# Kernel tuning notes

Measured on AMD Instinct MI355X. Metric: run time of the kernel, lower is better.

## Reference

```python
import jax, jax.numpy as jnp
import numpy as np

B, N, NFEAT = 32, 512, 256
NHID, NHEADS, NOUT = 64, 8, 128
ALPHA = 0.2    # GraphAttn LeakyReLU slope
ACVT_SLOPE = 0.01  # default nn.LeakyReLU slope in GAT.acvt
EPS = 1e-12


def _leaky(x, slope):
    return jnp.where(x >= 0, x, slope * x)


def setup_inputs() -> dict:
    key = jax.random.key(0)
    ks = jax.random.split(key, 10)
    s = lambda fan_in: 1.0 / np.sqrt(fan_in)
    return {
        "batch_descs": jax.random.normal(ks[0], (B, N, NFEAT), dtype=jnp.float32),
        # per-head GraphAttn params (nn.Linear weights, no bias)
        "W_tran": jax.random.uniform(ks[1], (NHEADS, NHID, NFEAT), jnp.float32, -s(NFEAT), s(NFEAT)),
        "a1": jax.random.uniform(ks[2], (NHEADS, NHID), jnp.float32, -s(NHID), s(NHID)),
        "a2": jax.random.uniform(ks[3], (NHEADS, NHID), jnp.float32, -s(NHID), s(NHID)),
        # output GraphAttn: in = NHID*NHEADS, out = NOUT
        "W_out": jax.random.uniform(ks[4], (NOUT, NHID * NHEADS), jnp.float32, -s(NHID * NHEADS), s(NHID * NHEADS)),
        "a1_out": jax.random.uniform(ks[5], (NOUT,), jnp.float32, -s(NOUT), s(NOUT)),
        "a2_out": jax.random.uniform(ks[6], (NOUT,), jnp.float32, -s(NOUT), s(NOUT)),
        # final nn.Linear(nout, nout) with bias
        "W_lin": jax.random.uniform(ks[7], (NOUT, NOUT), jnp.float32, -s(NOUT), s(NOUT)),
        "b_lin": jax.random.uniform(ks[8], (NOUT,), jnp.float32, -s(NOUT), s(NOUT)),
    }


def reference(batch_descs, W_tran, a1, a2, W_out, a1_out, a2_out, W_lin, b_lin):
    def gat_one_object(x):  # x: [N, NFEAT]; dense all-ones adj (ignored by GraphAttn)
        # ---- multi-head GraphAttn ----
        h = jnp.einsum('nf,hdf->hnd', x, W_tran)          # [H, N, NHID]
        e1 = jnp.einsum('hnd,hd->hn', h, a1)              # [H, N]
        e2 = jnp.einsum('hnd,hd->hn', h, a2)              # [H, N]
        # e[h, j, k] = a1(h_k) + a2(h_j); softmax over k (torch dim=1 on [N,N])
        e = _leaky(e1[:, None, :] + e2[:, :, None], ALPHA)  # [H, N, N]
        att = jax.nn.softmax(e, axis=-1)
        o = jnp.einsum('hjk,hkd->hjd', att, h)            # [H, N, NHID]
        o = jnp.transpose(o, (1, 0, 2)).reshape(N, NHEADS * NHID)  # concat heads
        # ---- acvt (dropout2 is identity in eval) ----
        x2 = _leaky(o, ACVT_SLOPE)
        # ---- output GraphAttn ----
        h2 = x2 @ W_out.T                                 # [N, NOUT]
        f1 = h2 @ a1_out                                  # [N]
        f2 = h2 @ a2_out                                  # [N]
        e_o = _leaky(f1[None, :] + f2[:, None], ALPHA)    # [N, N]
        att_o = jax.nn.softmax(e_o, axis=-1)
        out = att_o @ h2                                  # [N, NOUT]
        out = jnp.mean(out, axis=0)                       # [NOUT]
        return out @ W_lin.T + b_lin

    feats = jax.vmap(gat_one_object)(batch_descs)         # [B, NOUT]
    # F.normalize(p=2, dim=-1) with eps clamp
    norm = jnp.maximum(jnp.linalg.norm(feats, axis=-1, keepdims=True), EPS)
    return feats / norm
```

## Files before the change

kernel.cpp:

```cpp
#include <hip/hip_runtime.h>
#include <hip/hip_bf16.h>
#include <math.h>

#define ALPHA 0.2f
#define ACVT 0.01f

typedef __attribute__((ext_vector_type(8))) __bf16 bf16x8;
typedef __attribute__((ext_vector_type(4))) __bf16 bf16x4;
typedef __attribute__((ext_vector_type(4))) float f32x4;

__device__ __forceinline__ bf16x8 cvt8(const float* p) {
    float4 v0 = *(const float4*)p;
    float4 v1 = *(const float4*)(p + 4);
    bf16x8 o;
    o[0] = (__bf16)v0.x; o[1] = (__bf16)v0.y; o[2] = (__bf16)v0.z; o[3] = (__bf16)v0.w;
    o[4] = (__bf16)v1.x; o[5] = (__bf16)v1.y; o[6] = (__bf16)v1.z; o[7] = (__bf16)v1.w;
    return o;
}

__global__ __launch_bounds__(256) void gemm1_f(
    const float* __restrict__ X, const float* __restrict__ Wt,
    __bf16* __restrict__ HT,
    const float* __restrict__ a1, const float* __restrict__ a2,
    float* __restrict__ E1, float* __restrict__ E2) {
    __shared__ char As[128 * 128];
    __shared__ char Bs[128 * 128];
    __shared__ char Tt[128 * 264];
    const int tid = threadIdx.x;
    const int w = tid >> 6, lane = tid & 63;
    const int wm = w >> 1, wn = w & 1;
    const int r = lane & 15, g = lane >> 4;
    const int L = blockIdx.x;
    const int W = (L & 7) * 64 + (L >> 3);
    const int m_tile = W >> 2, n_tile = W & 3;
    const int m0 = m_tile * 128;
    const int n0 = n_tile * 128;

    f32x4 acc[4][4];
#pragma unroll
    for (int mt = 0; mt < 4; ++mt)
#pragma unroll
        for (int nt = 0; nt < 4; ++nt) {
            acc[mt][nt][0] = 0.f; acc[mt][nt][1] = 0.f;
            acc[mt][nt][2] = 0.f; acc[mt][nt][3] = 0.f;
        }

    const int sr = tid >> 3;
    const int c8 = (tid & 7) * 8;

    for (int k0 = 0; k0 < 256; k0 += 64) {
        __syncthreads();
#pragma unroll
        for (int i = 0; i < 4; ++i) {
            int row = sr + i * 32;
            bf16x8 va = cvt8(X + (size_t)(m0 + row) * 256 + k0 + c8);
            *(bf16x8*)(As + row * 128 + ((c8 * 2) ^ ((row & 7) << 4))) = va;
            bf16x8 vb = cvt8(Wt + (size_t)(n0 + row) * 256 + k0 + c8);
            *(bf16x8*)(Bs + row * 128 + ((c8 * 2) ^ ((row & 7) << 4))) = vb;
        }
        __syncthreads();
#pragma unroll
        for (int kk = 0; kk < 64; kk += 32) {
            bf16x8 af[4], bfv[4];
#pragma unroll
            for (int mt = 0; mt < 4; ++mt) {
                int row = wm * 64 + mt * 16 + r;
                af[mt] = *(const bf16x8*)(As + row * 128 +
                                          (((kk + g * 8) * 2) ^ ((row & 7) << 4)));
            }
#pragma unroll
            for (int nt = 0; nt < 4; ++nt) {
                int row = wn * 64 + nt * 16 + r;
                bfv[nt] = *(const bf16x8*)(Bs + row * 128 +
                                           (((kk + g * 8) * 2) ^ ((row & 7) << 4)));
            }
#pragma unroll
            for (int mt = 0; mt < 4; ++mt)
#pragma unroll
                for (int nt = 0; nt < 4; ++nt)
                    acc[mt][nt] = __builtin_amdgcn_mfma_f32_16x16x32_bf16(
                        af[mt], bfv[nt], acc[mt][nt], 0, 0, 0);
        }
    }

#pragma unroll
    for (int mt = 0; mt < 4; ++mt) {
        int node = wm * 64 + mt * 16 + g * 4;
#pragma unroll
        for (int nt = 0; nt < 4; ++nt) {
            int d_blk = wn * 64 + nt * 16 + r;
            bf16x4 pv;
#pragma unroll
            for (int reg = 0; reg < 4; ++reg) pv[reg] = (__bf16)acc[mt][nt][reg];
            *(bf16x4*)(Tt + d_blk * 264 + node * 2) = pv;
        }
    }
    __syncthreads();
    {
        const int b = m0 >> 9, nn = m0 & 511;
        const int h0 = n_tile * 2;
#pragma unroll
        for (int i = 0; i < 8; ++i) {
            int d_row = (tid >> 4) + i * 16;
            int hrow = (b * 8 + h0 + (d_row >> 6)) * 64 + (d_row & 63);
            bf16x8 v = *(const bf16x8*)(Tt + d_row * 264 + (tid & 15) * 16);
            *(bf16x8*)(HT + (size_t)hrow * 512 + nn + (tid & 15) * 8) = v;
        }
    }
    const int h = n_tile * 2 + wn;
    float w1[4], w2[4];
#pragma unroll
    for (int nt = 0; nt < 4; ++nt) {
        w1[nt] = a1[h * 64 + nt * 16 + r];
        w2[nt] = a2[h * 64 + nt * 16 + r];
    }
#pragma unroll
    for (int mt = 0; mt < 4; ++mt)
#pragma unroll
        for (int reg = 0; reg < 4; ++reg) {
            float s1 = 0.f, s2 = 0.f;
#pragma unroll
            for (int nt = 0; nt < 4; ++nt) {
                s1 += acc[mt][nt][reg] * w1[nt];
                s2 += acc[mt][nt][reg] * w2[nt];
            }
#pragma unroll
            for (int off = 1; off <= 8; off <<= 1) {
                s1 += __shfl_xor(s1, off, 64);
                s2 += __shfl_xor(s2, off, 64);
            }
            if (r == 0) {
                int m = m0 + wm * 64 + mt * 16 + g * 4 + reg;
                int b = m >> 9, n = m & 511;
                E1[(size_t)(b * 8 + h) * 512 + n] = s1;
                E2[(size_t)(b * 8 + h) * 512 + n] = s2;
            }
        }
}

__global__ __launch_bounds__(256) void attn_s(const __bf16* __restrict__ HT,
                                              const float* __restrict__ E1,
                                              const float* __restrict__ E2,
                                              __bf16* __restrict__ OL) {
    __shared__ char Hc[4096];
    __shared__ float e1s[512];
    __shared__ float redm[256];
    __shared__ float zrow[4][32];
    __shared__ float e1maxS;

    const int bid = blockIdx.x;
    const int bh = bid >> 2, qq = bid & 3;
    const int b = bh >> 3, h = bh & 7;
    const int tid = threadIdx.x;
    const int w = tid >> 6, lane = tid & 63;
    const int r = lane & 15, g = lane >> 4;

    for (int i = tid; i < 512; i += 256) e1s[i] = E1[(size_t)bh * 512 + i];
    __syncthreads();
    redm[tid] = fmaxf(e1s[tid], e1s[tid + 256]);
    __syncthreads();
    if (tid < 64) {
        float m = fmaxf(fmaxf(redm[tid], redm[tid + 64]),
                        fmaxf(redm[tid + 128], redm[tid + 192]));
#pragma unroll
        for (int off = 32; off >= 1; off >>= 1) m = fmaxf(m, __shfl_xor(m, off, 64));
        if (tid == 0) e1maxS = m;
    }
    __syncthreads();
    const float e1max = e1maxS;

    float ee2[2], mm[2];
    const float* e2g = E2 + (size_t)bh * 512 + qq * 128 + w * 32;
#pragma unroll
    for (int mt = 0; mt < 2; ++mt) {
        float v = e2g[mt * 16 + r];
        ee2[mt] = v;
        float s = e1max + v;
        mm[mt] = fmaxf(s, ALPHA * s);
    }

    f32x4 acc[2][4];
#pragma unroll
    for (int mt = 0; mt < 2; ++mt)
#pragma unroll
        for (int nt = 0; nt < 4; ++nt) {
            acc[mt][nt][0] = 0.f; acc[mt][nt][1] = 0.f;
            acc[mt][nt][2] = 0.f; acc[mt][nt][3] = 0.f;
        }
    float zac[2] = {0.f, 0.f};

    const int d_s = tid >> 2, kq = tid & 3;
    const __bf16* hsrc = HT + (size_t)(bh * 64 + d_s) * 512 + kq * 8;
    const int lw = d_s * 64 + ((kq * 16) ^ ((d_s & 3) << 4));
    bf16x8 stg = *(const bf16x8*)hsrc;

    for (int c = 0; c < 16; ++c) {
        __syncthreads();
        *(bf16x8*)(Hc + lw) = stg;
        __syncthreads();
        if (c < 15) stg = *(const bf16x8*)(hsrc + (c + 1) * 32);

        const float* ep = e1s + c * 32 + g * 8;
        float4 ea = *(const float4*)(ep);
        float4 eb = *(const float4*)(ep + 4);
        float e1c[8] = {ea.x, ea.y, ea.z, ea.w, eb.x, eb.y, eb.z, eb.w};

        bf16x8 bfr[4];
#pragma unroll
        for (int nt = 0; nt < 4; ++nt) {
            int d = nt * 16 + r;
            bfr[nt] = *(const bf16x8*)(Hc + d * 64 + ((g * 16) ^ ((d & 3) << 4)));
        }
#pragma unroll
        for (int mt = 0; mt < 2; ++mt) {
            bf16x8 af;
            float zp = 0.f;
#pragma unroll
            for (int q = 0; q < 8; ++q) {
                float s = e1c[q] + ee2[mt];
                s = fmaxf(s, ALPHA * s);
                float p = __expf(s - mm[mt]);
                zp += p;
                af[q] = (__bf16)p;
            }
            zac[mt] += zp;
#pragma unroll
            for (int nt = 0; nt < 4; ++nt)
                acc[mt][nt] =
                    __builtin_amdgcn_mfma_f32_16x16x32_bf16(af, bfr[nt], acc[mt][nt], 0, 0, 0);
        }
    }

#pragma unroll
    for (int mt = 0; mt < 2; ++mt) {
        float z = zac[mt];
        z += __shfl_xor(z, 16, 64);
        z += __shfl_xor(z, 32, 64);
        if (g == 0) zrow[w][mt * 16 + r] = 1.f / z;
    }

    __bf16* ob = OL + ((size_t)b * 512 + qq * 128 + w * 32) * 512 + h * 64;
#pragma unroll
    for (int mt = 0; mt < 2; ++mt) {
#pragma unroll
        for (int reg = 0; reg < 4; ++reg) {
            int row = mt * 16 + g * 4 + reg;
            float zi = zrow[w][row];
#pragma unroll
            for (int nt = 0; nt < 4; ++nt) {
                float v = acc[mt][nt][reg] * zi;
                v = fmaxf(v, ACVT * v);
                ob[(size_t)row * 512 + nt * 16 + r] = (__bf16)v;
            }
        }
    }
}

__global__ __launch_bounds__(256) void gemm2_f(
    const __bf16* __restrict__ OL, const float* __restrict__ Wo,
    __bf16* __restrict__ H2,
    const float* __restrict__ a1o, const float* __restrict__ a2o,
    float* __restrict__ F1, float* __restrict__ F2) {
    __shared__ char As[32 * 128];
    __shared__ char Bs[128 * 128];
    __shared__ float fred[2][32][2];
    const int tid = threadIdx.x;
    const int w = tid >> 6, lane = tid & 63;
    const int wm = w >> 1, wn = w & 1;
    const int r = lane & 15, g = lane >> 4;
    const int m0 = blockIdx.x * 32;

    f32x4 acc[4];
#pragma unroll
    for (int nt = 0; nt < 4; ++nt) {
        acc[nt][0] = 0.f; acc[nt][1] = 0.f; acc[nt][2] = 0.f; acc[nt][3] = 0.f;
    }

    const int sra = tid >> 3;
    const int c8 = (tid & 7) * 8;

    for (int k0 = 0; k0 < 512; k0 += 64) {
        __syncthreads();
        {
            bf16x8 va = *(const bf16x8*)((const char*)OL +
                                         ((size_t)(m0 + sra) * 512 + k0) * 2 + c8 * 2);
            *(bf16x8*)(As + sra * 128 + ((c8 * 2) ^ ((sra & 7) << 4))) = va;
        }
#pragma unroll
        for (int i = 0; i < 4; ++i) {
            int row = sra + i * 32;
            bf16x8 vb = cvt8(Wo + (size_t)row * 512 + k0 + c8);
            *(bf16x8*)(Bs + row * 128 + ((c8 * 2) ^ ((row & 7) << 4))) = vb;
        }
        __syncthreads();
#pragma unroll
        for (int kk = 0; kk < 64; kk += 32) {
            int arow = wm * 16 + r;
            bf16x8 af = *(const bf16x8*)(As + arow * 128 +
                                         (((kk + g * 8) * 2) ^ ((arow & 7) << 4)));
            bf16x8 bfv[4];
#pragma unroll
            for (int nt = 0; nt < 4; ++nt) {
                int row = wn * 64 + nt * 16 + r;
                bfv[nt] = *(const bf16x8*)(Bs + row * 128 +
                                           (((kk + g * 8) * 2) ^ ((row & 7) << 4)));
            }
#pragma unroll
            for (int nt = 0; nt < 4; ++nt)
                acc[nt] = __builtin_amdgcn_mfma_f32_16x16x32_bf16(af, bfv[nt], acc[nt], 0, 0, 0);
        }
    }

#pragma unroll
    for (int reg = 0; reg < 4; ++reg) {
        int row = m0 + wm * 16 + g * 4 + reg;
#pragma unroll
        for (int nt = 0; nt < 4; ++nt)
            H2[(size_t)row * 128 + wn * 64 + nt * 16 + r] = (__bf16)acc[nt][reg];
    }
    float w1[4], w2[4];
#pragma unroll
    for (int nt = 0; nt < 4; ++nt) {
        w1[nt] = a1o[wn * 64 + nt * 16 + r];
        w2[nt] = a2o[wn * 64 + nt * 16 + r];
    }
#pragma unroll
    for (int reg = 0; reg < 4; ++reg) {
        float s1 = 0.f, s2 = 0.f;
#pragma unroll
        for (int nt = 0; nt < 4; ++nt) {
            s1 += acc[nt][reg] * w1[nt];
            s2 += acc[nt][reg] * w2[nt];
        }
#pragma unroll
        for (int off = 1; off <= 8; off <<= 1) {
            s1 += __shfl_xor(s1, off, 64);
            s2 += __shfl_xor(s2, off, 64);
        }
        if (r == 0) {
            int lr = wm * 16 + g * 4 + reg;
            fred[wn][lr][0] = s1;
            fred[wn][lr][1] = s2;
        }
    }
    __syncthreads();
    if (tid < 32) {
        int m = m0 + tid;
        int b = m >> 9, n = m & 511;
        F1[(size_t)b * 512 + n] = fred[0][tid][0] + fred[1][tid][0];
        F2[(size_t)b * 512 + n] = fred[0][tid][1] + fred[1][tid][1];
    }
}

__global__ __launch_bounds__(256) void zw_k(const float* __restrict__ F1,
                                            const float* __restrict__ F2,
                                            float* __restrict__ WP) {
    __shared__ float f1s[512];
    __shared__ float wpart[4][512];
    __shared__ float redm[256];
    const int b = blockIdx.x >> 4, jc = blockIdx.x & 15;
    const int tid = threadIdx.x;
    const int w = tid >> 6, lane = tid & 63;

    f1s[tid] = F1[(size_t)b * 512 + tid];
    f1s[tid + 256] = F1[(size_t)b * 512 + tid + 256];
#pragma unroll
    for (int i = 0; i < 8; ++i) wpart[w][lane + 64 * i] = 0.f;
    __syncthreads();
    redm[tid] = fmaxf(f1s[tid], f1s[tid + 256]);
    __syncthreads();
    if (tid < 64) {
        float m = fmaxf(fmaxf(redm[tid], redm[tid + 64]), fmaxf(redm[tid + 128], redm[tid + 192]));
#pragma unroll
        for (int off = 32; off >= 1; off >>= 1) m = fmaxf(m, __shfl_xor(m, off, 64));
        if (tid == 0) redm[0] = m;
    }
    __syncthreads();
    const float f1m = redm[0];

    for (int jj = 0; jj < 8; ++jj) {
        int j = jc * 32 + w * 8 + jj;
        float f2j = F2[(size_t)b * 512 + j];
        float sj = f1m + f2j;
        float mj = fmaxf(sj, ALPHA * sj);
        float pv[8];
        float z = 0.f;
#pragma unroll
        for (int i = 0; i < 8; ++i) {
            float s = f1s[lane + 64 * i] + f2j;
            s = fmaxf(s, ALPHA * s);
            float p = __expf(s - mj);
            pv[i] = p;
            z += p;
        }
#pragma unroll
        for (int off = 32; off >= 1; off >>= 1) z += __shfl_xor(z, off, 64);
        float inv = 1.f / z;
#pragma unroll
        for (int i = 0; i < 8; ++i) wpart[w][lane + 64 * i] += pv[i] * inv;
    }
    __syncthreads();
    for (int i = tid; i < 512; i += 256)
        WP[(size_t)(b * 16 + jc) * 512 + i] =
            wpart[0][i] + wpart[1][i] + wpart[2][i] + wpart[3][i];
}

__global__ __launch_bounds__(512) void finalv_k(const float* __restrict__ WP,
                                                const __bf16* __restrict__ H2,
                                                const float* __restrict__ Wl,
                                                const float* __restrict__ bl,
                                                float* __restrict__ out) {
    __shared__ float wsL[512];
    __shared__ float part[4][128];
    __shared__ float vs[128];
    __shared__ float fo_s[128];
    __shared__ float r0;
    const int b = blockIdx.x, tid = threadIdx.x;
    {
        float s = 0.f;
#pragma unroll
        for (int jc = 0; jc < 16; ++jc) s += WP[(size_t)(b * 16 + jc) * 512 + tid];
        wsL[tid] = s;
    }
    __syncthreads();
    {
        const int q = tid >> 7, d = tid & 127;
        const __bf16* h2p = H2 + ((size_t)b * 512 + q * 128) * 128 + d;
        float acc = 0.f;
#pragma unroll 8
        for (int i = 0; i < 128; ++i) acc += wsL[q * 128 + i] * (float)h2p[(size_t)i * 128];
        part[q][d] = acc;
    }
    __syncthreads();
    if (tid < 128)
        vs[tid] = (part[0][tid] + part[1][tid] + part[2][tid] + part[3][tid]) * (1.f / 512.f);
    __syncthreads();
    if (tid < 128) {
        float fo = bl[tid];
        const float* wl = Wl + (size_t)tid * 128;
#pragma unroll 4
        for (int d = 0; d < 128; d += 4)
            fo += vs[d] * wl[d] + vs[d + 1] * wl[d + 1] + vs[d + 2] * wl[d + 2] +
                  vs[d + 3] * wl[d + 3];
        fo_s[tid] = fo;
    }
    __syncthreads();
    if (tid < 64) {
        float s = fo_s[tid] * fo_s[tid] + fo_s[tid + 64] * fo_s[tid + 64];
#pragma unroll
        for (int off = 32; off >= 1; off >>= 1) s += __shfl_xor(s, off, 64);
        if (tid == 0) r0 = s;
    }
    __syncthreads();
    float inv = 1.f / fmaxf(sqrtf(r0), 1e-12f);
    if (tid < 128) out[(size_t)b * 128 + tid] = fo_s[tid] * inv;
}

extern "C" void kernel_launch(void* const* d_in, const int* in_sizes, int n_in,
                              void* d_out, int out_size, void* d_ws, size_t ws_size,
                              hipStream_t stream) {
    const float* X = (const float*)d_in[0];
    const float* Wt = (const float*)d_in[1];
    const float* a1 = (const float*)d_in[2];
    const float* a2 = (const float*)d_in[3];
    const float* Wo = (const float*)d_in[4];
    const float* a1o = (const float*)d_in[5];
    const float* a2o = (const float*)d_in[6];
    const float* Wl = (const float*)d_in[7];
    const float* bl = (const float*)d_in[8];
    float* out = (float*)d_out;

    char* p = (char*)d_ws;
    __bf16* HT = (__bf16*)p;  p += (size_t)8388608 * 2;
    __bf16* OL = (__bf16*)p;  p += (size_t)8388608 * 2;
    float* E1 = (float*)p;    p += (size_t)131072 * 4;
    float* E2 = (float*)p;    p += (size_t)131072 * 4;
    __bf16* H2 = (__bf16*)p;  p += (size_t)2097152 * 2;
    float* F1 = (float*)p;    p += (size_t)16384 * 4;
    float* F2 = (float*)p;    p += (size_t)16384 * 4;
    float* WP = (float*)p;    p += (size_t)262144 * 4;

    gemm1_f<<<512, 256, 0, stream>>>(X, Wt, HT, a1, a2, E1, E2);
    attn_s<<<1024, 256, 0, stream>>>(HT, E1, E2, OL);
    gemm2_f<<<512, 256, 0, stream>>>(OL, Wo, H2, a1o, a2o, F1, F2);
    zw_k<<<512, 256, 0, stream>>>(F1, F2, WP);
    finalv_k<<<32, 512, 0, stream>>>(WP, H2, Wl, bl, out);
}
```

Before: 143.6 us.

## Fuse multi-head attention with output projection, split heads into partial sums

Merges the per-head attention kernel and the second GEMM into one kernel. Each block handles 64 query rows for four heads, and the activated attention output goes through LDS straight into an MFMA against Wo, so the 16 MB OL intermediate is never written to or read from global memory. The two head halves write partial H2, F1 and F2 buffers that the later kernels add together. H fragments now load directly from global into registers instead of being staged in LDS. Costs: the grid drops from 1024 to 512 blocks, Wo is re-converted per head, and the downstream kernels read twice as much partial data.

```diff
diff --git a/kernel.cpp b/kernel.cpp
--- a/kernel.cpp
+++ b/kernel.cpp
@@ -138,199 +138,154 @@
         }
 }
 
-__global__ __launch_bounds__(256) void attn_s(const __bf16* __restrict__ HT,
-                                              const float* __restrict__ E1,
-                                              const float* __restrict__ E2,
-                                              __bf16* __restrict__ OL) {
-    __shared__ char Hc[4096];
-    __shared__ float e1s[512];
-    __shared__ float redm[256];
-    __shared__ float zrow[4][32];
-    __shared__ float e1maxS;
+__global__ __launch_bounds__(256) void attnfused(
+    const __bf16* __restrict__ HT, const float* __restrict__ E1,
+    const float* __restrict__ E2, const float* __restrict__ Wo,
+    const float* __restrict__ a1o, const float* __restrict__ a2o,
+    __bf16* __restrict__ H2P, float* __restrict__ F1P, float* __restrict__ F2P) {
+    __shared__ char Wos[128 * 128];
+    __shared__ float e1s[4][512];
+    __shared__ char pbuf[4][2048];
+    __shared__ float e1mx[4];
+    __shared__ float zrow[4][16];
 
     const int bid = blockIdx.x;
-    const int bh = bid >> 2, qq = bid & 3;
-    const int b = bh >> 3, h = bh & 7;
+    const int b = bid >> 4, e8 = (bid >> 1) & 7, hh2 = bid & 1;
+    const int j0 = e8 * 64;
     const int tid = threadIdx.x;
     const int w = tid >> 6, lane = tid & 63;
     const int r = lane & 15, g = lane >> 4;
 
-    for (int i = tid; i < 512; i += 256) e1s[i] = E1[(size_t)bh * 512 + i];
-    __syncthreads();
-    redm[tid] = fmaxf(e1s[tid], e1s[tid + 256]);
-    __syncthreads();
-    if (tid < 64) {
-        float m = fmaxf(fmaxf(redm[tid], redm[tid + 64]),
-                        fmaxf(redm[tid + 128], redm[tid + 192]));
+    for (int i = tid; i < 2048; i += 256) {
+        int hh = i >> 9;
+        e1s[hh][i & 511] = E1[((size_t)(b * 8 + hh2 * 4 + hh)) * 512 + (i & 511)];
+    }
+    __syncthreads();
+    {
+        float m = -1e30f;
+#pragma unroll
+        for (int i = 0; i < 8; ++i) m = fmaxf(m, e1s[w][lane + 64 * i]);
 #pragma unroll
         for (int off = 32; off >= 1; off >>= 1) m = fmaxf(m, __shfl_xor(m, off, 64));
-        if (tid == 0) e1maxS = m;
-    }
-    __syncthreads();
-    const float e1max = e1maxS;
-
-    float ee2[2], mm[2];
-    const float* e2g = E2 + (size_t)bh * 512 + qq * 128 + w * 32;
-#pragma unroll
-    for (int mt = 0; mt < 2; ++mt) {
-        float v = e2g[mt * 16 + r];
-        ee2[mt] = v;
-        float s = e1max + v;
-        mm[mt] = fmaxf(s, ALPHA * s);
-    }
-
-    f32x4 acc[2][4];
-#pragma unroll
-    for (int mt = 0; mt < 2; ++mt)
+        if (lane == 0) e1mx[w] = m;
+    }
+
+    f32x4 h2acc[8];
+#pragma unroll
+    for (int ct = 0; ct < 8; ++ct) {
+        h2acc[ct][0] = 0.f; h2acc[ct][1] = 0.f; h2acc[ct][2] = 0.f; h2acc[ct][3] = 0.f;
+    }
+
+    const int row_j = j0 + w * 16 + r;
+    char* pb = pbuf[w];
+
+    for (int hh = 0; hh < 4; ++hh) {
+        const int h = hh2 * 4 + hh;
+        const size_t bh = (size_t)b * 8 + h;
+        __syncthreads();
+        {
+            int c = tid >> 1, dh = tid & 1;
+            const float* wsrc = Wo + (size_t)c * 512 + h * 64 + dh * 32;
+#pragma unroll
+            for (int q = 0; q < 4; ++q) {
+                bf16x8 v = cvt8(wsrc + q * 8);
+                *(bf16x8*)(Wos + c * 128 + (((dh * 32 + q * 8) * 2) ^ ((c & 7) << 4))) = v;
+            }
+        }
+        __syncthreads();
+
+        const float ee2 = E2[bh * 512 + row_j];
+        float mml;
+        { float s = e1mx[hh] + ee2; mml = fmaxf(s, ALPHA * s); }
+
+        f32x4 acc[4];
 #pragma unroll
         for (int nt = 0; nt < 4; ++nt) {
-            acc[mt][nt][0] = 0.f; acc[mt][nt][1] = 0.f;
-            acc[mt][nt][2] = 0.f; acc[mt][nt][3] = 0.f;
-        }
-    float zac[2] = {0.f, 0.f};
-
-    const int d_s = tid >> 2, kq = tid & 3;
-    const __bf16* hsrc = HT + (size_t)(bh * 64 + d_s) * 512 + kq * 8;
-    const int lw = d_s * 64 + ((kq * 16) ^ ((d_s & 3) << 4));
-    bf16x8 stg = *(const bf16x8*)hsrc;
-
-    for (int c = 0; c < 16; ++c) {
-        __syncthreads();
-        *(bf16x8*)(Hc + lw) = stg;
-        __syncthreads();
-        if (c < 15) stg = *(const bf16x8*)(hsrc + (c + 1) * 32);
-
-        const float* ep = e1s + c * 32 + g * 8;
-        float4 ea = *(const float4*)(ep);
-        float4 eb = *(const float4*)(ep + 4);
-        float e1c[8] = {ea.x, ea.y, ea.z, ea.w, eb.x, eb.y, eb.z, eb.w};
-
-        bf16x8 bfr[4];
-#pragma unroll
-        for (int nt = 0; nt < 4; ++nt) {
-            int d = nt * 16 + r;
-            bfr[nt] = *(const bf16x8*)(Hc + d * 64 + ((g * 16) ^ ((d & 3) << 4)));
-        }
-#pragma unroll
-        for (int mt = 0; mt < 2; ++mt) {
+            acc[nt][0] = 0.f; acc[nt][1] = 0.f; acc[nt][2] = 0.f; acc[nt][3] = 0.f;
+        }
+        float zac = 0.f;
+
+        const __bf16* hb = HT + bh * 32768;
+        bf16x8 cur[4], nxt[4];
+#pragma unroll
+        for (int nt = 0; nt < 4; ++nt)
+            cur[nt] = *(const bf16x8*)(hb + (size_t)(nt * 16 + r) * 512 + g * 8);
+
+        for (int c = 0; c < 16; ++c) {
+            if (c < 15) {
+#pragma unroll
+                for (int nt = 0; nt < 4; ++nt)
+                    nxt[nt] = *(const bf16x8*)(hb + (size_t)(nt * 16 + r) * 512 +
+                                               (c + 1) * 32 + g * 8);
+            }
+            const float* ep = &e1s[hh][c * 32 + g * 8];
+            float4 ea = *(const float4*)(ep);
+            float4 eb = *(const float4*)(ep + 4);
+            float e1c[8] = {ea.x, ea.y, ea.z, ea.w, eb.x, eb.y, eb.z, eb.w};
             bf16x8 af;
             float zp = 0.f;
 #pragma unroll
             for (int q = 0; q < 8; ++q) {
-                float s = e1c[q] + ee2[mt];
+                float s = e1c[q] + ee2;
                 s = fmaxf(s, ALPHA * s);
-                float p = __expf(s - mm[mt]);
+                float p = __expf(s - mml);
                 zp += p;
                 af[q] = (__bf16)p;
             }
-            zac[mt] += zp;
+            zac += zp;
 #pragma unroll
             for (int nt = 0; nt < 4; ++nt)
-                acc[mt][nt] =
-                    __builtin_amdgcn_mfma_f32_16x16x32_bf16(af, bfr[nt], acc[mt][nt], 0, 0, 0);
-        }
-    }
-
-#pragma unroll
-    for (int mt = 0; mt < 2; ++mt) {
-        float z = zac[mt];
+                acc[nt] = __builtin_amdgcn_mfma_f32_16x16x32_bf16(af, cur[nt], acc[nt], 0, 0, 0);
+            if (c < 15) {
+#pragma unroll
+                for (int nt = 0; nt < 4; ++nt) cur[nt] = nxt[nt];
+            }
+        }
+
+        float z = zac;
         z += __shfl_xor(z, 16, 64);
         z += __shfl_xor(z, 32, 64);
-        if (g == 0) zrow[w][mt * 16 + r] = 1.f / z;
-    }
-
-    __bf16* ob = OL + ((size_t)b * 512 + qq * 128 + w * 32) * 512 + h * 64;
-#pragma unroll
-    for (int mt = 0; mt < 2; ++mt) {
+        if (g == 0) zrow[w][r] = 1.f / z;
+
 #pragma unroll
         for (int reg = 0; reg < 4; ++reg) {
-            int row = mt * 16 + g * 4 + reg;
+            int row = g * 4 + reg;
             float zi = zrow[w][row];
 #pragma unroll
             for (int nt = 0; nt < 4; ++nt) {
-                float v = acc[mt][nt][reg] * zi;
+                float v = acc[nt][reg] * zi;
                 v = fmaxf(v, ACVT * v);
-                ob[(size_t)row * 512 + nt * 16 + r] = (__bf16)v;
-            }
-        }
-    }
-}
-
-__global__ __launch_bounds__(256) void gemm2_f(
-    const __bf16* __restrict__ OL, const float* __restrict__ Wo,
-    __bf16* __restrict__ H2,
-    const float* __restrict__ a1o, const float* __restrict__ a2o,
-    float* __restrict__ F1, float* __restrict__ F2) {
-    __shared__ char As[32 * 128];
-    __shared__ char Bs[128 * 128];
-    __shared__ float fred[2][32][2];
-    const int tid = threadIdx.x;
-    const int w = tid >> 6, lane = tid & 63;
-    const int wm = w >> 1, wn = w & 1;
-    const int r = lane & 15, g = lane >> 4;
-    const int m0 = blockIdx.x * 32;
-
-    f32x4 acc[4];
-#pragma unroll
-    for (int nt = 0; nt < 4; ++nt) {
-        acc[nt][0] = 0.f; acc[nt][1] = 0.f; acc[nt][2] = 0.f; acc[nt][3] = 0.f;
-    }
-
-    const int sra = tid >> 3;
-    const int c8 = (tid & 7) * 8;
-
-    for (int k0 = 0; k0 < 512; k0 += 64) {
-        __syncthreads();
-        {
-            bf16x8 va = *(const bf16x8*)((const char*)OL +
-                                         ((size_t)(m0 + sra) * 512 + k0) * 2 + c8 * 2);
-            *(bf16x8*)(As + sra * 128 + ((c8 * 2) ^ ((sra & 7) << 4))) = va;
-        }
-#pragma unroll
-        for (int i = 0; i < 4; ++i) {
-            int row = sra + i * 32;
-            bf16x8 vb = cvt8(Wo + (size_t)row * 512 + k0 + c8);
-            *(bf16x8*)(Bs + row * 128 + ((c8 * 2) ^ ((row & 7) << 4))) = vb;
-        }
-        __syncthreads();
-#pragma unroll
-        for (int kk = 0; kk < 64; kk += 32) {
-            int arow = wm * 16 + r;
-            bf16x8 af = *(const bf16x8*)(As + arow * 128 +
-                                         (((kk + g * 8) * 2) ^ ((arow & 7) << 4)));
-            bf16x8 bfv[4];
-#pragma unroll
-            for (int nt = 0; nt < 4; ++nt) {
-                int row = wn * 64 + nt * 16 + r;
-                bfv[nt] = *(const bf16x8*)(Bs + row * 128 +
-                                           (((kk + g * 8) * 2) ^ ((row & 7) << 4)));
-            }
-#pragma unroll
-            for (int nt = 0; nt < 4; ++nt)
-                acc[nt] = __builtin_amdgcn_mfma_f32_16x16x32_bf16(af, bfv[nt], acc[nt], 0, 0, 0);
-        }
-    }
-
-#pragma unroll
-    for (int reg = 0; reg < 4; ++reg) {
-        int row = m0 + wm * 16 + g * 4 + reg;
-#pragma unroll
-        for (int nt = 0; nt < 4; ++nt)
-            H2[(size_t)row * 128 + wn * 64 + nt * 16 + r] = (__bf16)acc[nt][reg];
-    }
-    float w1[4], w2[4];
-#pragma unroll
-    for (int nt = 0; nt < 4; ++nt) {
-        w1[nt] = a1o[wn * 64 + nt * 16 + r];
-        w2[nt] = a2o[wn * 64 + nt * 16 + r];
+                *(__bf16*)(pb + ((row * 128 + (nt * 16 + r) * 2) ^ ((row & 7) << 4))) =
+                    (__bf16)v;
+            }
+        }
+#pragma unroll
+        for (int ks = 0; ks < 2; ++ks) {
+            bf16x8 pa = *(const bf16x8*)(pb + ((r * 128 + (ks * 32 + g * 8) * 2) ^
+                                               ((r & 7) << 4)));
+#pragma unroll
+            for (int ct = 0; ct < 8; ++ct) {
+                int cc = ct * 16 + r;
+                bf16x8 wf = *(const bf16x8*)(Wos + cc * 128 +
+                                             (((ks * 32 + g * 8) * 2) ^ ((cc & 7) << 4)));
+                h2acc[ct] = __builtin_amdgcn_mfma_f32_16x16x32_bf16(pa, wf, h2acc[ct], 0, 0, 0);
+            }
+        }
+    }
+
+    float w1[8], w2[8];
+#pragma unroll
+    for (int ct = 0; ct < 8; ++ct) {
+        w1[ct] = a1o[ct * 16 + r];
+        w2[ct] = a2o[ct * 16 + r];
     }
 #pragma unroll
     for (int reg = 0; reg < 4; ++reg) {
         float s1 = 0.f, s2 = 0.f;
 #pragma unroll
-        for (int nt = 0; nt < 4; ++nt) {
-            s1 += acc[nt][reg] * w1[nt];
-            s2 += acc[nt][reg] * w2[nt];
+        for (int ct = 0; ct < 8; ++ct) {
+            s1 += h2acc[ct][reg] * w1[ct];
+            s2 += h2acc[ct][reg] * w2[ct];
         }
 #pragma unroll
         for (int off = 1; off <= 8; off <<= 1) {
@@ -338,32 +293,33 @@
             s2 += __shfl_xor(s2, off, 64);
         }
         if (r == 0) {
-            int lr = wm * 16 + g * 4 + reg;
-            fred[wn][lr][0] = s1;
-            fred[wn][lr][1] = s2;
-        }
-    }
-    __syncthreads();
-    if (tid < 32) {
-        int m = m0 + tid;
-        int b = m >> 9, n = m & 511;
-        F1[(size_t)b * 512 + n] = fred[0][tid][0] + fred[1][tid][0];
-        F2[(size_t)b * 512 + n] = fred[0][tid][1] + fred[1][tid][1];
-    }
-}
-
-__global__ __launch_bounds__(256) void zw_k(const float* __restrict__ F1,
-                                            const float* __restrict__ F2,
+            int m = b * 512 + j0 + w * 16 + g * 4 + reg;
+            F1P[hh2 * 16384 + m] = s1;
+            F2P[hh2 * 16384 + m] = s2;
+        }
+    }
+    __bf16* hp = H2P + (size_t)hh2 * 2097152 + ((size_t)b * 512 + j0 + w * 16) * 128;
+#pragma unroll
+    for (int reg = 0; reg < 4; ++reg)
+#pragma unroll
+        for (int ct = 0; ct < 8; ++ct)
+            hp[(size_t)(g * 4 + reg) * 128 + ct * 16 + r] = (__bf16)h2acc[ct][reg];
+}
+
+__global__ __launch_bounds__(256) void zw_k(const float* __restrict__ F1P,
+                                            const float* __restrict__ F2P,
                                             float* __restrict__ WP) {
-    __shared__ float f1s[512];
+    __shared__ float f1s[512], f2s[512];
     __shared__ float wpart[4][512];
     __shared__ float redm[256];
     const int b = blockIdx.x >> 4, jc = blockIdx.x & 15;
     const int tid = threadIdx.x;
     const int w = tid >> 6, lane = tid & 63;
 
-    f1s[tid] = F1[(size_t)b * 512 + tid];
-    f1s[tid + 256] = F1[(size_t)b * 512 + tid + 256];
+    for (int i = tid; i < 512; i += 256) {
+        f1s[i] = F1P[(size_t)b * 512 + i] + F1P[16384 + (size_t)b * 512 + i];
+        f2s[i] = F2P[(size_t)b * 512 + i] + F2P[16384 + (size_t)b * 512 + i];
+    }
 #pragma unroll
     for (int i = 0; i < 8; ++i) wpart[w][lane + 64 * i] = 0.f;
     __syncthreads();
@@ -380,7 +336,7 @@
 
     for (int jj = 0; jj < 8; ++jj) {
         int j = jc * 32 + w * 8 + jj;
-        float f2j = F2[(size_t)b * 512 + j];
+        float f2j = f2s[j];
         float sj = f1m + f2j;
         float mj = fmaxf(sj, ALPHA * sj);
         float pv[8];
@@ -406,7 +362,7 @@
 }
 
 __global__ __launch_bounds__(512) void finalv_k(const float* __restrict__ WP,
-                                                const __bf16* __restrict__ H2,
+                                                const __bf16* __restrict__ H2P,
                                                 const float* __restrict__ Wl,
                                                 const float* __restrict__ bl,
                                                 float* __restrict__ out) {
@@ -425,10 +381,13 @@
     __syncthreads();
     {
         const int q = tid >> 7, d = tid & 127;
-        const __bf16* h2p = H2 + ((size_t)b * 512 + q * 128) * 128 + d;
+        const __bf16* h2p = H2P + ((size_t)b * 512 + q * 128) * 128 + d;
+        const __bf16* h2q = h2p + 2097152;
         float acc = 0.f;
 #pragma unroll 8
-        for (int i = 0; i < 128; ++i) acc += wsL[q * 128 + i] * (float)h2p[(size_t)i * 128];
+        for (int i = 0; i < 128; ++i)
+            acc += wsL[q * 128 + i] *
+                   ((float)h2p[(size_t)i * 128] + (float)h2q[(size_t)i * 128]);
         part[q][d] = acc;
     }
     __syncthreads();
@@ -472,17 +431,15 @@
 
     char* p = (char*)d_ws;
     __bf16* HT = (__bf16*)p;  p += (size_t)8388608 * 2;
-    __bf16* OL = (__bf16*)p;  p += (size_t)8388608 * 2;
     float* E1 = (float*)p;    p += (size_t)131072 * 4;
     float* E2 = (float*)p;    p += (size_t)131072 * 4;
-    __bf16* H2 = (__bf16*)p;  p += (size_t)2097152 * 2;
-    float* F1 = (float*)p;    p += (size_t)16384 * 4;
-    float* F2 = (float*)p;    p += (size_t)16384 * 4;
+    __bf16* H2P = (__bf16*)p; p += (size_t)2 * 2097152 * 2;
+    float* F1P = (float*)p;   p += (size_t)2 * 16384 * 4;
+    float* F2P = (float*)p;   p += (size_t)2 * 16384 * 4;
     float* WP = (float*)p;    p += (size_t)262144 * 4;
 
     gemm1_f<<<512, 256, 0, stream>>>(X, Wt, HT, a1, a2, E1, E2);
-    attn_s<<<1024, 256, 0, stream>>>(HT, E1, E2, OL);
-    gemm2_f<<<512, 256, 0, stream>>>(OL, Wo, H2, a1o, a2o, F1, F2);
-    zw_k<<<512, 256, 0, stream>>>(F1, F2, WP);
-    finalv_k<<<32, 512, 0, stream>>>(WP, H2, Wl, bl, out);
-}
+    attnfused<<<512, 256, 0, stream>>>(HT, E1, E2, Wo, a1o, a2o, H2P, F1P, F2P);
+    zw_k<<<512, 256, 0, stream>>>(F1P, F2P, WP);
+    finalv_k<<<32, 512, 0, stream>>>(WP, H2P, Wl, bl, out);
+}
```

After: 178.6 us. 24.3% more time.
